# Kernel optimization log

Measured on AMD Instinct MI355X. Metric: run time of the kernel, lower is better.

Reference implementation:

```python
import jax, jax.numpy as jnp
import numpy as np

IN_F = 8192
OUT_F = 8192
R = 16
LORA_ALPHA = 32
BLOCK = 64
SCALING = LORA_ALPHA / R  # 2.0
NUMEL = IN_F * OUT_F


def dequantize_4bit(packed, scales):
    # packed: [numel//2] bytes (stored as int32 in [0,255]); element 2i = low nibble, 2i+1 = high nibble
    low = packed & 0xF
    high = (packed >> 4) & 0xF
    q = jnp.stack([low, high], axis=-1).reshape(-1)          # [numel] ints in [0,15]
    flat = q.astype(jnp.float32) - 8.0                        # signed 4-bit
    flat = (flat.reshape(-1, BLOCK) * scales[:, None]).reshape(-1)  # blockwise scale
    return flat.reshape(OUT_F, IN_F)


def setup_inputs() -> dict:
    key = jax.random.key(0)
    k1, k2, k3, k4, k5 = jax.random.split(key, 5)
    x = jax.random.normal(k1, (1, 64, IN_F), dtype=jnp.float32)
    packed_weights = jax.random.randint(k2, (NUMEL // 2,), 0, 256, dtype=jnp.int32)
    block_scales = jax.random.uniform(k3, (NUMEL // BLOCK,), dtype=jnp.float32) * 0.05
    # kaiming_uniform(a=sqrt(5)) on [R, IN_F] -> bound = 1/sqrt(IN_F)
    bound = 1.0 / np.sqrt(IN_F)
    lora_A = jax.random.uniform(k4, (R, IN_F), minval=-bound, maxval=bound, dtype=jnp.float32)
    # original init is zeros; use small randn for a non-trivial baseline
    lora_B = jax.random.normal(k5, (OUT_F, R), dtype=jnp.float32) * 0.02
    return {"x": x, "packed_weights": packed_weights, "block_scales": block_scales,
            "lora_A": lora_A, "lora_B": lora_B}


def reference(x, packed_weights, block_scales, lora_A, lora_B):
    W = dequantize_4bit(packed_weights, block_scales).astype(x.dtype)  # [OUT_F, IN_F]
    base_out = jnp.einsum('bsi,oi->bso', x, W)                         # no bias (bias_buffer=None)
    lora_out = jnp.einsum('bsr,or->bso', jnp.einsum('bsi,ri->bsr', x, lora_A), lora_B) * SCALING
    return base_out + lora_out
```

## Files before the change

kernel.cpp:

```cpp
#include <hip/hip_runtime.h>
#include <hip/hip_bf16.h>

#define IN_F 8192
#define OUT_F 8192
#define SEQ 64
#define LORA_R 16
#define KH 4096

typedef __attribute__((ext_vector_type(4))) float f32x4;
typedef __attribute__((ext_vector_type(4))) int i32x4;
typedef __attribute__((ext_vector_type(8))) unsigned short u16x8;
typedef _Float16 f16x2 __attribute__((ext_vector_type(2)));
typedef _Float16 f16x8 __attribute__((ext_vector_type(8)));

__global__ __launch_bounds__(256) void k_cast(const float* __restrict__ x,
                                              unsigned short* __restrict__ xb) {
    const int i = (blockIdx.x * 256 + threadIdx.x) * 8;
    f32x4 v0 = *(const f32x4*)(x + i);
    f32x4 v1 = *(const f32x4*)(x + i + 4);
    u16x8 h;
    h[0] = __builtin_bit_cast(unsigned short, (_Float16)v0.x);
    h[1] = __builtin_bit_cast(unsigned short, (_Float16)v0.y);
    h[2] = __builtin_bit_cast(unsigned short, (_Float16)v0.z);
    h[3] = __builtin_bit_cast(unsigned short, (_Float16)v0.w);
    h[4] = __builtin_bit_cast(unsigned short, (_Float16)v1.x);
    h[5] = __builtin_bit_cast(unsigned short, (_Float16)v1.y);
    h[6] = __builtin_bit_cast(unsigned short, (_Float16)v1.z);
    h[7] = __builtin_bit_cast(unsigned short, (_Float16)v1.w);
    *(u16x8*)(xb + i) = h;
}

__global__ __launch_bounds__(512) void k_t(const float* __restrict__ x,
                                           const float* __restrict__ A,
                                           float* __restrict__ t) {
    __shared__ float p[LORA_R][33];
    const int s = blockIdx.x;
    const int r = threadIdx.x & 15, seg = threadIdx.x >> 4;
    const float* xr = x + s * IN_F + seg * 256;
    const float* ar = A + r * IN_F + seg * 256;
    float acc = 0.f;
    #pragma unroll 8
    for (int j = 0; j < 64; ++j) {
        f32x4 xv = *(const f32x4*)(xr + j * 4);
        f32x4 av = *(const f32x4*)(ar + j * 4);
        acc = fmaf(xv.x, av.x, acc);
        acc = fmaf(xv.y, av.y, acc);
        acc = fmaf(xv.z, av.z, acc);
        acc = fmaf(xv.w, av.w, acc);
    }
    p[r][seg] = acc;
    __syncthreads();
    if (threadIdx.x < LORA_R) {
        float v = 0.f;
        #pragma unroll
        for (int g = 0; g < 32; ++g) v += p[threadIdx.x][g];
        t[s * LORA_R + threadIdx.x] = v;
    }
}

__global__ __launch_bounds__(512, 4) void k_main(
    const int* __restrict__ packed, const float* __restrict__ scales,
    const unsigned short* __restrict__ xb, const float* __restrict__ t,
    const float* __restrict__ B, float* __restrict__ out) {
    __shared__ char lds[60928];
    _Float16* xs = (_Float16*)lds;
    int* wt = (int*)(lds + 34816);
    float* scs = (float*)(lds + 52224);
    float* accs = (float*)lds;

    const int tid = threadIdx.x;
    const int n0 = (blockIdx.x >> 1) * 32;
    const int kh = blockIdx.x & 1;
    const int w = tid >> 6, lane = tid & 63;
    const int nh = w >> 2, wkk = w & 3;
    const int q = lane >> 4, c16 = lane & 15;

    {
        int row = tid >> 4, g = tid & 15;
        f32x4 v = *(const f32x4*)(scales + (n0 + row) * (IN_F / 64) + kh * 64 + g * 4);
        *(f32x4*)(scs + row * 68 + g * 4) = v;
    }

    const int xrow = tid >> 3, xseg = tid & 7;
    const int wrow = tid >> 4, wg = tid & 15;
    const unsigned short* xsrc = xb + xrow * IN_F + kh * KH + xseg * 16;
    const int* wsrc = packed + (long)(n0 + wrow) * (IN_F / 2) + kh * (KH / 2) + wg * 4;
    _Float16* xdst0 = xs + xrow * 136 + xseg * 16;
    int* wdst0 = wt + wrow * 68 + wg * 4;

    f32x4 acc[4];
    #pragma unroll
    for (int mt = 0; mt < 4; ++mt) acc[mt] = (f32x4){0.f, 0.f, 0.f, 0.f};

    const f16x2 c1032 = {(_Float16)1032.0f, (_Float16)1032.0f};

    auto compute = [&](int buf, int kt) {
        i32x4 pv = *(const i32x4*)(wt + buf * (32 * 68) + (nh * 16 + c16) * 68 + wkk * 16 + q * 4);
        float scf = scs[(nh * 16 + c16) * 68 + kt * 2 + (wkk >> 1)];
        _Float16 sch = (_Float16)scf;
        f16x2 sc2 = {sch, sch};
        f16x8 bf;
        #pragma unroll
        for (int m = 0; m < 4; ++m) {
            unsigned u = ((((unsigned)pv[m] << 12) | (unsigned)pv[m]) & 0x000F000Fu) | 0x64006400u;
            f16x2 h = __builtin_bit_cast(f16x2, u);
            h = (h - c1032) * sc2;
            bf[2 * m] = h.x;
            bf[2 * m + 1] = h.y;
        }
        const _Float16* xbase = xs + buf * (64 * 136) + wkk * 32 + q * 8;
        #pragma unroll
        for (int mt = 0; mt < 4; ++mt) {
            f16x8 af = *(const f16x8*)(xbase + (mt * 16 + c16) * 136);
            acc[mt] = __builtin_amdgcn_mfma_f32_16x16x32_f16(af, bf, acc[mt], 0, 0, 0);
        }
    };

    u16x8 a0 = *(const u16x8*)(xsrc);
    u16x8 b0 = *(const u16x8*)(xsrc + 8);
    i32x4 w0 = *(const i32x4*)(wsrc);
    *(u16x8*)xdst0 = a0;
    *(u16x8*)(xdst0 + 8) = b0;
    *(i32x4*)wdst0 = w0;
    u16x8 a1 = *(const u16x8*)(xsrc + 128);
    u16x8 b1 = *(const u16x8*)(xsrc + 128 + 8);
    i32x4 w1 = *(const i32x4*)(wsrc + 64);
    __syncthreads();

    for (int kt = 0; kt < 32; kt += 2) {
        if (kt + 2 < 32) {
            a0 = *(const u16x8*)(xsrc + (kt + 2) * 128);
            b0 = *(const u16x8*)(xsrc + (kt + 2) * 128 + 8);
            w0 = *(const i32x4*)(wsrc + (kt + 2) * 64);
        }
        compute(0, kt);
        *(u16x8*)(xs + 64 * 136 + xrow * 136 + xseg * 16) = a1;
        *(u16x8*)(xs + 64 * 136 + xrow * 136 + xseg * 16 + 8) = b1;
        *(i32x4*)(wt + 32 * 68 + wrow * 68 + wg * 4) = w1;
        __syncthreads();
        if (kt + 3 < 32) {
            a1 = *(const u16x8*)(xsrc + (kt + 3) * 128);
            b1 = *(const u16x8*)(xsrc + (kt + 3) * 128 + 8);
            w1 = *(const i32x4*)(wsrc + (kt + 3) * 64);
        }
        compute(1, kt + 1);
        if (kt + 2 < 32) {
            *(u16x8*)xdst0 = a0;
            *(u16x8*)(xdst0 + 8) = b0;
            *(i32x4*)wdst0 = w0;
            __syncthreads();
        }
    }
    __syncthreads();

    float* myacc = accs + w * (64 * 17);
    #pragma unroll
    for (int mt = 0; mt < 4; ++mt)
        #pragma unroll
        for (int r = 0; r < 4; ++r)
            myacc[(mt * 16 + q * 4 + r) * 17 + c16] = acc[mt][r];
    __syncthreads();

    #pragma unroll
    for (int j = 0; j < 4; ++j) {
        int p = tid + j * 512;
        int s = p >> 5, c = p & 31;
        const float* ab = accs + (c >> 4) * 4 * (64 * 17) + s * 17 + (c & 15);
        float v = ab[0] + ab[64 * 17] + ab[2 * 64 * 17] + ab[3 * 64 * 17];
        if (kh == 0) {
            const float* tp = t + s * LORA_R;
            const float* bp = B + (n0 + c) * LORA_R;
            float lr = 0.f;
            #pragma unroll
            for (int r = 0; r < LORA_R; ++r) lr = fmaf(tp[r], bp[r], lr);
            v += 2.0f * lr;
        }
        unsafeAtomicAdd(&out[s * OUT_F + n0 + c], v);
    }
}

extern "C" void kernel_launch(void* const* d_in, const int* in_sizes, int n_in,
                              void* d_out, int out_size, void* d_ws, size_t ws_size,
                              hipStream_t stream) {
    const float* x      = (const float*)d_in[0];
    const int* packed   = (const int*)d_in[1];
    const float* scales = (const float*)d_in[2];
    const float* lora_A = (const float*)d_in[3];
    const float* lora_B = (const float*)d_in[4];
    float* out = (float*)d_out;

    unsigned short* xb = (unsigned short*)d_ws;
    float* t = (float*)((char*)d_ws + (size_t)SEQ * IN_F * 2);

    hipMemsetAsync(out, 0, (size_t)SEQ * OUT_F * sizeof(float), stream);
    k_cast<<<SEQ * IN_F / (256 * 8), 256, 0, stream>>>(x, xb);
    k_t<<<SEQ, 512, 0, stream>>>(x, lora_A, t);
    k_main<<<512, 512, 0, stream>>>(packed, scales, xb, t, lora_B, out);
}
```

Before: 239.9 us.

## Fuse cast, LoRA projection and output zeroing into one prep kernel; simplify pipeline

Merges the fp16 cast of x, the LoRA x·A^T projection and the output zero-fill into a single prep kernel, removing a memset and two launches. The main GEMM loop becomes a single-stage prefetch with two barriers per k-step instead of the manually unrolled two-register-set pipeline. Weight loads now use nontemporal hints to avoid polluting cache with streamed data. The shallower prefetch and extra barrier per iteration may expose more memory latency.

```diff
diff --git a/kernel.cpp b/kernel.cpp
--- a/kernel.cpp
+++ b/kernel.cpp
@@ -10,51 +10,50 @@
 typedef __attribute__((ext_vector_type(4))) float f32x4;
 typedef __attribute__((ext_vector_type(4))) int i32x4;
 typedef __attribute__((ext_vector_type(8))) unsigned short u16x8;
+typedef __attribute__((ext_vector_type(4))) unsigned short u16x4;
 typedef _Float16 f16x2 __attribute__((ext_vector_type(2)));
 typedef _Float16 f16x8 __attribute__((ext_vector_type(8)));
 
-__global__ __launch_bounds__(256) void k_cast(const float* __restrict__ x,
-                                              unsigned short* __restrict__ xb) {
-    const int i = (blockIdx.x * 256 + threadIdx.x) * 8;
-    f32x4 v0 = *(const f32x4*)(x + i);
-    f32x4 v1 = *(const f32x4*)(x + i + 4);
-    u16x8 h;
-    h[0] = __builtin_bit_cast(unsigned short, (_Float16)v0.x);
-    h[1] = __builtin_bit_cast(unsigned short, (_Float16)v0.y);
-    h[2] = __builtin_bit_cast(unsigned short, (_Float16)v0.z);
-    h[3] = __builtin_bit_cast(unsigned short, (_Float16)v0.w);
-    h[4] = __builtin_bit_cast(unsigned short, (_Float16)v1.x);
-    h[5] = __builtin_bit_cast(unsigned short, (_Float16)v1.y);
-    h[6] = __builtin_bit_cast(unsigned short, (_Float16)v1.z);
-    h[7] = __builtin_bit_cast(unsigned short, (_Float16)v1.w);
-    *(u16x8*)(xb + i) = h;
-}
+__global__ __launch_bounds__(512) void k_prep(
+    const float* __restrict__ x, const float* __restrict__ A,
+    unsigned short* __restrict__ xb, float* __restrict__ t,
+    float* __restrict__ out) {
+    const int tid = threadIdx.x;
+    const int gi = blockIdx.x * 512 + tid;
 
-__global__ __launch_bounds__(512) void k_t(const float* __restrict__ x,
-                                           const float* __restrict__ A,
-                                           float* __restrict__ t) {
-    __shared__ float p[LORA_R][33];
-    const int s = blockIdx.x;
-    const int r = threadIdx.x & 15, seg = threadIdx.x >> 4;
-    const float* xr = x + s * IN_F + seg * 256;
-    const float* ar = A + r * IN_F + seg * 256;
-    float acc = 0.f;
-    #pragma unroll 8
-    for (int j = 0; j < 64; ++j) {
-        f32x4 xv = *(const f32x4*)(xr + j * 4);
-        f32x4 av = *(const f32x4*)(ar + j * 4);
-        acc = fmaf(xv.x, av.x, acc);
-        acc = fmaf(xv.y, av.y, acc);
-        acc = fmaf(xv.z, av.z, acc);
-        acc = fmaf(xv.w, av.w, acc);
-    }
-    p[r][seg] = acc;
-    __syncthreads();
-    if (threadIdx.x < LORA_R) {
-        float v = 0.f;
-        #pragma unroll
-        for (int g = 0; g < 32; ++g) v += p[threadIdx.x][g];
-        t[s * LORA_R + threadIdx.x] = v;
+    f32x4 v = *(const f32x4*)(x + gi * 4);
+    u16x4 h;
+    h[0] = __builtin_bit_cast(unsigned short, (_Float16)v.x);
+    h[1] = __builtin_bit_cast(unsigned short, (_Float16)v.y);
+    h[2] = __builtin_bit_cast(unsigned short, (_Float16)v.z);
+    h[3] = __builtin_bit_cast(unsigned short, (_Float16)v.w);
+    *(u16x4*)(xb + gi * 4) = h;
+    *(f32x4*)(out + gi * 4) = (f32x4){0.f, 0.f, 0.f, 0.f};
+
+    if (blockIdx.x < SEQ) {
+        __shared__ float p[LORA_R][33];
+        const int s = blockIdx.x;
+        const int r = tid & 15, seg = tid >> 4;
+        const float* xr = x + s * IN_F + seg * 256;
+        const float* ar = A + r * IN_F + seg * 256;
+        float acc = 0.f;
+        #pragma unroll 8
+        for (int j = 0; j < 64; ++j) {
+            f32x4 xv = *(const f32x4*)(xr + j * 4);
+            f32x4 av = *(const f32x4*)(ar + j * 4);
+            acc = fmaf(xv.x, av.x, acc);
+            acc = fmaf(xv.y, av.y, acc);
+            acc = fmaf(xv.z, av.z, acc);
+            acc = fmaf(xv.w, av.w, acc);
+        }
+        p[r][seg] = acc;
+        __syncthreads();
+        if (tid < LORA_R) {
+            float sum = 0.f;
+            #pragma unroll
+            for (int g = 0; g < 32; ++g) sum += p[tid][g];
+            t[s * LORA_R + tid] = sum;
+        }
     }
 }
 
@@ -94,8 +93,25 @@
 
     const f16x2 c1032 = {(_Float16)1032.0f, (_Float16)1032.0f};
 
-    auto compute = [&](int buf, int kt) {
-        i32x4 pv = *(const i32x4*)(wt + buf * (32 * 68) + (nh * 16 + c16) * 68 + wkk * 16 + q * 4);
+    {
+        u16x8 a0 = *(const u16x8*)(xsrc);
+        u16x8 b0 = *(const u16x8*)(xsrc + 8);
+        i32x4 w0 = __builtin_nontemporal_load((const i32x4*)wsrc);
+        *(u16x8*)xdst0 = a0;
+        *(u16x8*)(xdst0 + 8) = b0;
+        *(i32x4*)wdst0 = w0;
+    }
+    __syncthreads();
+
+    for (int kt = 0; kt < 32; ++kt) {
+        const int cur = kt & 1;
+        u16x8 ga, gb; i32x4 gw;
+        if (kt < 31) {
+            ga = *(const u16x8*)(xsrc + (kt + 1) * 128);
+            gb = *(const u16x8*)(xsrc + (kt + 1) * 128 + 8);
+            gw = __builtin_nontemporal_load((const i32x4*)(wsrc + (kt + 1) * 64));
+        }
+        i32x4 pv = *(const i32x4*)(wt + cur * (32 * 68) + (nh * 16 + c16) * 68 + wkk * 16 + q * 4);
         float scf = scs[(nh * 16 + c16) * 68 + kt * 2 + (wkk >> 1)];
         _Float16 sch = (_Float16)scf;
         f16x2 sc2 = {sch, sch};
@@ -103,55 +119,25 @@
         #pragma unroll
         for (int m = 0; m < 4; ++m) {
             unsigned u = ((((unsigned)pv[m] << 12) | (unsigned)pv[m]) & 0x000F000Fu) | 0x64006400u;
-            f16x2 h = __builtin_bit_cast(f16x2, u);
-            h = (h - c1032) * sc2;
-            bf[2 * m] = h.x;
-            bf[2 * m + 1] = h.y;
+            f16x2 hh = __builtin_bit_cast(f16x2, u);
+            hh = (hh - c1032) * sc2;
+            bf[2 * m] = hh.x;
+            bf[2 * m + 1] = hh.y;
         }
-        const _Float16* xbase = xs + buf * (64 * 136) + wkk * 32 + q * 8;
+        const _Float16* xbase = xs + cur * (64 * 136) + wkk * 32 + q * 8;
         #pragma unroll
         for (int mt = 0; mt < 4; ++mt) {
             f16x8 af = *(const f16x8*)(xbase + (mt * 16 + c16) * 136);
             acc[mt] = __builtin_amdgcn_mfma_f32_16x16x32_f16(af, bf, acc[mt], 0, 0, 0);
         }
-    };
-
-    u16x8 a0 = *(const u16x8*)(xsrc);
-    u16x8 b0 = *(const u16x8*)(xsrc + 8);
-    i32x4 w0 = *(const i32x4*)(wsrc);
-    *(u16x8*)xdst0 = a0;
-    *(u16x8*)(xdst0 + 8) = b0;
-    *(i32x4*)wdst0 = w0;
-    u16x8 a1 = *(const u16x8*)(xsrc + 128);
-    u16x8 b1 = *(const u16x8*)(xsrc + 128 + 8);
-    i32x4 w1 = *(const i32x4*)(wsrc + 64);
-    __syncthreads();
-
-    for (int kt = 0; kt < 32; kt += 2) {
-        if (kt + 2 < 32) {
-            a0 = *(const u16x8*)(xsrc + (kt + 2) * 128);
-            b0 = *(const u16x8*)(xsrc + (kt + 2) * 128 + 8);
-            w0 = *(const i32x4*)(wsrc + (kt + 2) * 64);
+        __syncthreads();
+        if (kt < 31) {
+            *(u16x8*)(xs + (1 - cur) * (64 * 136) + xrow * 136 + xseg * 16)     = ga;
+            *(u16x8*)(xs + (1 - cur) * (64 * 136) + xrow * 136 + xseg * 16 + 8) = gb;
+            *(i32x4*)(wt + (1 - cur) * (32 * 68) + wrow * 68 + wg * 4)          = gw;
         }
-        compute(0, kt);
-        *(u16x8*)(xs + 64 * 136 + xrow * 136 + xseg * 16) = a1;
-        *(u16x8*)(xs + 64 * 136 + xrow * 136 + xseg * 16 + 8) = b1;
-        *(i32x4*)(wt + 32 * 68 + wrow * 68 + wg * 4) = w1;
         __syncthreads();
-        if (kt + 3 < 32) {
-            a1 = *(const u16x8*)(xsrc + (kt + 3) * 128);
-            b1 = *(const u16x8*)(xsrc + (kt + 3) * 128 + 8);
-            w1 = *(const i32x4*)(wsrc + (kt + 3) * 64);
-        }
-        compute(1, kt + 1);
-        if (kt + 2 < 32) {
-            *(u16x8*)xdst0 = a0;
-            *(u16x8*)(xdst0 + 8) = b0;
-            *(i32x4*)wdst0 = w0;
-            __syncthreads();
-        }
     }
-    __syncthreads();
 
     float* myacc = accs + w * (64 * 17);
     #pragma unroll
@@ -192,8 +178,6 @@
     unsigned short* xb = (unsigned short*)d_ws;
     float* t = (float*)((char*)d_ws + (size_t)SEQ * IN_F * 2);
 
-    hipMemsetAsync(out, 0, (size_t)SEQ * OUT_F * sizeof(float), stream);
-    k_cast<<<SEQ * IN_F / (256 * 8), 256, 0, stream>>>(x, xb);
-    k_t<<<SEQ, 512, 0, stream>>>(x, lora_A, t);
+    k_prep<<<256, 512, 0, stream>>>(x, lora_A, xb, t, out);
     k_main<<<512, 512, 0, stream>>>(packed, scales, xb, t, lora_B, out);
 }
```

New measurement: 234.9 us. -2.1%, faster.
